# Optimization experiments

Hardware: AMD Instinct MI355X
Metric: run time of the kernel (lower is better)

Reference implementation:

```python
import jax, jax.numpy as jnp
import numpy as np

H, KV, HD = 16, 8, 128           # heads, kv heads, head_dim
THETA, EPS = 1.0e6, 1e-6         # rope theta, rmsnorm eps
QMAX = 127.0                     # symmetric int8


def qdq(x):
    """Symmetric int8 fake quant-dequant along last dim (per-token / per-out-channel)."""
    s = jnp.maximum(jnp.max(jnp.abs(x), axis=-1, keepdims=True) / QMAX, 1e-8)
    q = jnp.clip(jnp.round(x / s), -QMAX, QMAX) * s
    return x + jax.lax.stop_gradient(q - x)  # STE


def rms_norm(x, w):
    v = jnp.mean(jnp.square(x.astype(jnp.float32)), axis=-1, keepdims=True)
    return (x.astype(jnp.float32) * jax.lax.rsqrt(v + EPS)).astype(x.dtype) * w


def rotate_half(x):
    x1, x2 = jnp.split(x, 2, axis=-1)
    return jnp.concatenate([-x2, x1], axis=-1)


def setup_inputs() -> dict:
    key = jax.random.key(0)
    ks = jax.random.split(key, 6)
    B, S, D = 1, 2048, 2048
    return {
        "hidden_states": jax.random.normal(ks[0], (B, S, D), jnp.float32),
        "Wq": jax.random.normal(ks[1], (H * HD, D), jnp.float32) * 0.02,
        "Wk": jax.random.normal(ks[2], (KV * HD, D), jnp.float32) * 0.02,
        "Wv": jax.random.normal(ks[3], (KV * HD, D), jnp.float32) * 0.02,
        "Wo": jax.random.normal(ks[4], (D, H * HD), jnp.float32) * 0.02,
        "q_norm_w": jnp.ones((HD,), jnp.float32),
        "k_norm_w": jnp.ones((HD,), jnp.float32),
        "position_ids": jnp.arange(S, dtype=jnp.int32)[None, :],
    }


def reference(hidden_states, Wq, Wk, Wv, Wo, q_norm_w, k_norm_w, position_ids):
    B, S, D = hidden_states.shape
    xq = qdq(hidden_states)                                  # per-token act quant (shared input)
    q = (xq @ qdq(Wq).T).reshape(B, S, H, HD).transpose(0, 2, 1, 3)   # [B,H,S,hd]
    k = (xq @ qdq(Wk).T).reshape(B, S, KV, HD).transpose(0, 2, 1, 3)  # [B,KV,S,hd]
    v = (xq @ qdq(Wv).T).reshape(B, S, KV, HD).transpose(0, 2, 1, 3)

    q = rms_norm(q, q_norm_w)
    k = rms_norm(k, k_norm_w)

    # rotary embeddings
    inv = 1.0 / (THETA ** (jnp.arange(0, HD, 2, dtype=jnp.float32) / HD))
    freqs = position_ids.astype(jnp.float32)[..., None] * inv          # [B,S,hd/2]
    emb = jnp.concatenate([freqs, freqs], axis=-1)                     # [B,S,hd]
    cos = jnp.cos(emb)[:, None].astype(q.dtype)                        # [B,1,S,hd]
    sin = jnp.sin(emb)[:, None].astype(q.dtype)
    q = q * cos + rotate_half(q) * sin
    k = k * cos + rotate_half(k) * sin

    # qkt_matmul.quant_x1 / quant_x2
    q = qdq(q)
    k = qdq(k)

    # GQA repeat
    g = H // KV
    k = jnp.repeat(k, g, axis=1)
    v = jnp.repeat(v, g, axis=1)

    scores = jnp.einsum("bhqd,bhkd->bhqk", q, k) * (HD ** -0.5)       # [B,H,S,S]
    causal = jnp.tril(jnp.ones((S, S), bool))
    scores = jnp.where(causal[None, None], scores, jnp.float32(-1e9))
    p = jax.nn.softmax(scores.astype(jnp.float32), axis=-1).astype(q.dtype)

    # pv_matmul.quant_x1 / quant_x2
    p = qdq(p)
    v = qdq(v)
    attn = jnp.einsum("bhqk,bhkd->bhqd", p, v)                        # [B,H,S,hd]
    attn = attn.transpose(0, 2, 1, 3).reshape(B, S, H * HD)
    return qdq(attn) @ qdq(Wo).T
```

## Files before the change

kernel.cpp:

```cpp
#include <hip/hip_runtime.h>
#include <math.h>

#define NH 16
#define NKV 8
#define HDIM 128
#define SEQ 2048
#define DMODEL 2048

typedef int   v4i __attribute__((ext_vector_type(4)));
typedef float v4f __attribute__((ext_vector_type(4)));
typedef _Float16 v8h __attribute__((ext_vector_type(8)));

static constexpr float SM_SCALE = 0.08838834764831843f;

#define GLOBP(p) (__attribute__((address_space(1))) void*)(p)
#define LDSP(p)  (__attribute__((address_space(3))) void*)(p)
#define ASYNC16(g, l) __builtin_amdgcn_global_load_lds(GLOBP(g), LDSP(l), 16, 0, 0)


__device__ __forceinline__ unsigned short f2h_bits(float x) {
    _Float16 h = (_Float16)x;
    return __builtin_bit_cast(unsigned short, h);
}

__global__ __launch_bounds__(256) void quant_rope_k(const float* __restrict__ hidden,
        const float* __restrict__ Wq, const float* __restrict__ Wk,
        const float* __restrict__ Wv, const float* __restrict__ Wo,
        const int* __restrict__ pos_ids,
        signed char* __restrict__ out, float* __restrict__ scale,
        float* __restrict__ ct, float* __restrict__ st) {
    int p = blockIdx.x;
    if (p >= 512) {
        int t = (p - 512) * 4 + (threadIdx.x >> 6);
        int fi = threadIdx.x & 63;
        float inv = 1.0f / (float)pow(1.0e6, (double)fi / 64.0);
        float fr = (float)pos_ids[t] * inv;
        float sn, c;
        sincosf(fr, &sn, &c);
        ct[t * 64 + fi] = c;
        st[t * 64 + fi] = sn;
        return;
    }
    int row0g = p * 16;
    const float* in; int lr0;
    if (row0g < 2048)      { in = hidden; lr0 = row0g; }
    else if (row0g < 4096) { in = Wq; lr0 = row0g - 2048; }
    else if (row0g < 5120) { in = Wk; lr0 = row0g - 4096; }
    else if (row0g < 6144) { in = Wv; lr0 = row0g - 5120; }
    else                   { in = Wo; lr0 = row0g - 6144; }
    const int cols = 2048;
    int tid = threadIdx.x;
    __shared__ float srow[16];
    int r = tid >> 4, l16 = tid & 15;
    const float4* x4 = (const float4*)(in + (size_t)(lr0 + r) * cols);
    float amax = 0.f;
    for (int c4 = l16; c4 < (cols >> 2); c4 += 16) {
        float4 v = x4[c4];
        amax = fmaxf(amax, fmaxf(fmaxf(fabsf(v.x), fabsf(v.y)),
                                 fmaxf(fabsf(v.z), fabsf(v.w))));
    }
#pragma unroll
    for (int m = 1; m <= 8; m <<= 1) amax = fmaxf(amax, __shfl_xor(amax, m));
    if (l16 == 0) {
        float s = fmaxf(amax / 127.0f, 1e-8f);
        srow[r] = s;
        scale[row0g + r] = s;
    }
    __syncthreads();
    int total = (cols >> 4) * 16;
    size_t obase = (size_t)p * 32768;
    for (int idx = tid; idx < total; idx += 256) {
        int f = idx >> 6, q = (idx >> 4) & 3, rr = idx & 15;
        const float* src = in + (size_t)(lr0 + rr) * cols + f * 64 + q * 16;
        float s = srow[rr];
        unsigned int wds[4];
#pragma unroll
        for (int g = 0; g < 4; ++g) {
            float4 v = *(const float4*)(src + g * 4);
            int b0 = (int)fminf(fmaxf(rintf(v.x / s), -127.f), 127.f);
            int b1 = (int)fminf(fmaxf(rintf(v.y / s), -127.f), 127.f);
            int b2 = (int)fminf(fmaxf(rintf(v.z / s), -127.f), 127.f);
            int b3 = (int)fminf(fmaxf(rintf(v.w / s), -127.f), 127.f);
            wds[g] = (b0 & 255) | ((b1 & 255) << 8) | ((b2 & 255) << 16) | ((b3 & 255) << 24);
        }
        *(uint4*)(out + obase + (size_t)idx * 16) =
            make_uint4(wds[0], wds[1], wds[2], wds[3]);
    }
}

__global__ __launch_bounds__(256) void row_quant_red_k(const float* __restrict__ attn2,
        const float* __restrict__ pp, const float* __restrict__ zb,
        signed char* __restrict__ out, float* __restrict__ scale) {
    int row0 = blockIdx.x * 16;
    int tid = threadIdx.x;
    __shared__ float srow[16];
    __shared__ float4 spvt[16][17];
    {
        int r = tid >> 4, h = tid & 15;
        int row = row0 + r;
        int t32 = row >> 6, rr = row & 63;
        const float2* zb2 = (const float2*)zb;
        float2 a0 = zb2[(((size_t)h * 32 + t32) * 2 + 0) * 64 + rr];
        float2 a1 = zb2[(((size_t)h * 32 + t32) * 2 + 1) * 64 + rr];
        float M = fmaxf(a0.x, a1.x);
        float w0 = __expf(a0.x - M), w1 = __expf(a1.x - M);
        float Zt = a0.y * w0 + a1.y * w1;
        float spv = fmaxf((1.0f / Zt) / 127.0f, 1e-8f);
        spvt[r][h] = make_float4(w0, w1, spv, 0.f);
    }
    __syncthreads();
    int r = tid >> 4, l16 = tid & 15;
    int row = row0 + r;
    const float4* x4 = (const float4*)(attn2 + (size_t)row * 2048);
    size_t ppr = ((size_t)(row >> 6) * 64 + (row & 63)) * 128;
    float amax = 0.f;
    for (int c4 = l16; c4 < 512; c4 += 16) {
        float4 v = x4[c4];
        int h = c4 >> 5;
        int j = (c4 & 31) * 4;
        float4 pv = *(const float4*)&pp[(size_t)h * 32 * 64 * 128 + ppr + j];
        float4 wz = spvt[r][h];
        v.x = (v.x * wz.x + pv.x * wz.y) * wz.z;
        v.y = (v.y * wz.x + pv.y * wz.y) * wz.z;
        v.z = (v.z * wz.x + pv.z * wz.y) * wz.z;
        v.w = (v.w * wz.x + pv.w * wz.y) * wz.z;
        amax = fmaxf(amax, fmaxf(fmaxf(fabsf(v.x), fabsf(v.y)),
                                 fmaxf(fabsf(v.z), fabsf(v.w))));
    }
#pragma unroll
    for (int m = 1; m <= 8; m <<= 1) amax = fmaxf(amax, __shfl_xor(amax, m));
    if (l16 == 0) {
        float s = fmaxf(amax / 127.0f, 1e-8f);
        srow[r] = s;
        scale[row0 + r] = s;
    }
    __syncthreads();
    size_t obase = ((size_t)(row0 >> 4) * 32) << 10;
    for (int idx = tid; idx < 2048; idx += 256) {
        int f = idx >> 6, q = (idx >> 4) & 3, rr16 = idx & 15;
        int rowb = row0 + rr16;
        int colb = f * 64 + q * 16;
        const float* src = attn2 + (size_t)rowb * 2048 + colb;
        float s = srow[rr16];
        int h = f >> 1;
        float4 wz = spvt[rr16][h];
        size_t ppb = (size_t)h * 32 * 64 * 128
                   + ((size_t)(rowb >> 6) * 64 + (rowb & 63)) * 128 + (colb & 127);
        unsigned int wds[4];
#pragma unroll
        for (int g = 0; g < 4; ++g) {
            float4 v = *(const float4*)(src + g * 4);
            float4 pv = *(const float4*)&pp[ppb + g * 4];
            v.x = (v.x * wz.x + pv.x * wz.y) * wz.z;
            v.y = (v.y * wz.x + pv.y * wz.y) * wz.z;
            v.z = (v.z * wz.x + pv.z * wz.y) * wz.z;
            v.w = (v.w * wz.x + pv.w * wz.y) * wz.z;
            int b0 = (int)fminf(fmaxf(rintf(v.x / s), -127.f), 127.f);
            int b1 = (int)fminf(fmaxf(rintf(v.y / s), -127.f), 127.f);
            int b2 = (int)fminf(fmaxf(rintf(v.z / s), -127.f), 127.f);
            int b3 = (int)fminf(fmaxf(rintf(v.w / s), -127.f), 127.f);
            wds[g] = (b0 & 255) | ((b1 & 255) << 8) | ((b2 & 255) << 16) | ((b3 & 255) << 24);
        }
        *(uint4*)(out + obase + (size_t)idx * 16) =
            make_uint4(wds[0], wds[1], wds[2], wds[3]);
    }
}

__global__ __launch_bounds__(256, 3) void gemm_o_k(const signed char* __restrict__ A,
        const float* __restrict__ sa, const signed char* __restrict__ B,
        const float* __restrict__ sb, float* __restrict__ C, int M, int N, int K) {
    __shared__ __align__(16) signed char lsA[3][8192];
    __shared__ __align__(16) signed char lsB[3][4096];
    int tid = threadIdx.x;
    int w = tid >> 6, l = tid & 63;
    int wr = w >> 1, wc = w & 1;
    int lrow = l & 15;
    int m0 = blockIdx.y * 128, n0 = blockIdx.x * 64;
    int kb6 = K >> 6;
    v4i acc[4][2];
#pragma unroll
    for (int i = 0; i < 4; ++i)
#pragma unroll
        for (int j = 0; j < 2; ++j) acc[i][j] = (v4i){0, 0, 0, 0};

    auto stage = [&](int buf, int k6) {
#pragma unroll
        for (int a = 0; a < 2; ++a) {
            int f = a * 4 + w;
            ASYNC16(A + (((size_t)(((m0 >> 4) + f) * kb6 + k6)) << 10) + l * 16,
                    lsA[buf] + f * 1024);
        }
        ASYNC16(B + (((size_t)(((n0 >> 4) + w) * kb6 + k6)) << 10) + l * 16,
                lsB[buf] + w * 1024);
    };

    stage(0, 0);
    if (kb6 > 1) {
        stage(1, 1);
        asm volatile("s_waitcnt vmcnt(3)" ::: "memory");
    } else {
        asm volatile("s_waitcnt vmcnt(0)" ::: "memory");
    }
    __builtin_amdgcn_s_barrier();
    for (int t = 0; t < kb6; ++t) {
        if (t + 2 < kb6) stage((t + 2) % 3, t + 2);
        int cur = t % 3;
        v4i af[4], bf[2];
#pragma unroll
        for (int i = 0; i < 4; ++i) af[i] = *(const v4i*)(lsA[cur] + (wr * 4 + i) * 1024 + l * 16);
#pragma unroll
        for (int j = 0; j < 2; ++j) bf[j] = *(const v4i*)(lsB[cur] + (wc * 2 + j) * 1024 + l * 16);
#pragma unroll
        for (int i = 0; i < 4; ++i)
#pragma unroll
            for (int j = 0; j < 2; ++j)
                acc[i][j] = __builtin_amdgcn_mfma_i32_16x16x64_i8(af[i], bf[j], acc[i][j], 0, 0, 0);
        if (t + 2 < kb6) asm volatile("s_waitcnt vmcnt(3)" ::: "memory");
        else             asm volatile("s_waitcnt vmcnt(0)" ::: "memory");
        __builtin_amdgcn_s_barrier();
    }
    int r0 = m0 + wr * 64, c0 = n0 + wc * 32;
    int lg = l >> 4;
    float sbv[2];
#pragma unroll
    for (int j = 0; j < 2; ++j) sbv[j] = sb[c0 + j * 16 + lrow];
#pragma unroll
    for (int i = 0; i < 4; ++i) {
        float4 s4 = *(const float4*)(sa + r0 + i * 16 + lg * 4);
        float sav[4] = {s4.x, s4.y, s4.z, s4.w};
#pragma unroll
        for (int j = 0; j < 2; ++j) {
#pragma unroll
            for (int reg = 0; reg < 4; ++reg) {
                int rr = r0 + i * 16 + lg * 4 + reg;
                C[(size_t)rr * N + c0 + j * 16 + lrow] = (float)acc[i][j][reg] * (sav[reg] * sbv[j]);
            }
        }
    }
}

__global__ __launch_bounds__(256, 2) void gemm_qkv_k(const signed char* __restrict__ A,
        const float* __restrict__ sa, const signed char* __restrict__ B,
        const float* __restrict__ sb,
        const float* __restrict__ qw, const float* __restrict__ kw,
        const float* __restrict__ ct, const float* __restrict__ st,
        signed char* __restrict__ q_i8, float* __restrict__ sq,
        signed char* __restrict__ k_i8, float* __restrict__ sk,
        unsigned short* __restrict__ vtT) {
    __shared__ __align__(16) char smem[68608];
    signed char (*lsA)[8192] = (signed char(*)[8192])smem;
    signed char (*lsB)[8192] = (signed char(*)[8192])(smem + 24576);
    float (*tile)[132] = (float(*)[132])smem;
    float* srow = (float*)(smem + 67584);
    int tid = threadIdx.x;
    int w = tid >> 6, l = tid & 63;
    int wr = w >> 1, wc = w & 1;
    int lrow = l & 15, lg = l >> 4;
    int m0 = blockIdx.y * 128, n0 = blockIdx.x * 128;
    const int kb6 = 32;
    v4i acc[4][4];
#pragma unroll
    for (int i = 0; i < 4; ++i)
#pragma unroll
        for (int j = 0; j < 4; ++j) acc[i][j] = (v4i){0, 0, 0, 0};

    auto stage = [&](int buf, int k6) {
#pragma unroll
        for (int a = 0; a < 2; ++a) {
            int f = a * 4 + w;
            ASYNC16(A + (((size_t)(((m0 >> 4) + f) * kb6 + k6)) << 10) + l * 16,
                    lsA[buf] + f * 1024);
            ASYNC16(B + (((size_t)(((n0 >> 4) + f) * kb6 + k6)) << 10) + l * 16,
                    lsB[buf] + f * 1024);
        }
    };

    stage(0, 0);
    stage(1, 1);
    asm volatile("s_waitcnt vmcnt(4)" ::: "memory");
    __builtin_amdgcn_s_barrier();
    for (int t = 0; t < kb6; ++t) {
        if (t + 2 < kb6) stage((t + 2) % 3, t + 2);
        int cur = t % 3;
        v4i af[4], bf[4];
#pragma unroll
        for (int i = 0; i < 4; ++i) af[i] = *(const v4i*)(lsA[cur] + (wr * 4 + i) * 1024 + l * 16);
#pragma unroll
        for (int j = 0; j < 4; ++j) bf[j] = *(const v4i*)(lsB[cur] + (wc * 4 + j) * 1024 + l * 16);
#pragma unroll
        for (int i = 0; i < 4; ++i)
#pragma unroll
            for (int j = 0; j < 4; ++j)
                acc[i][j] = __builtin_amdgcn_mfma_i32_16x16x64_i8(af[i], bf[j], acc[i][j], 0, 0, 0);
        if (t + 2 < kb6) asm volatile("s_waitcnt vmcnt(4)" ::: "memory");
        else             asm volatile("s_waitcnt vmcnt(0)" ::: "memory");
        __builtin_amdgcn_s_barrier();
    }
    {
        int c0 = n0 + wc * 64;
        float sbv[4];
#pragma unroll
        for (int j = 0; j < 4; ++j) sbv[j] = sb[c0 + j * 16 + lrow];
#pragma unroll
        for (int i = 0; i < 4; ++i) {
            float4 s4 = *(const float4*)(sa + m0 + wr * 64 + i * 16 + lg * 4);
            float sav[4] = {s4.x, s4.y, s4.z, s4.w};
#pragma unroll
            for (int j = 0; j < 4; ++j)
#pragma unroll
                for (int reg = 0; reg < 4; ++reg)
                    tile[wr * 64 + i * 16 + lg * 4 + reg][wc * 64 + j * 16 + lrow] =
                        (float)acc[i][j][reg] * (sav[reg] * sbv[j]);
        }
    }
    __syncthreads();
    int slot = n0 >> 7;
    if (slot < 24) {
        const float* wn = (slot < 16) ? qw : kw;
        signed char* dst8 = (slot < 16) ? q_i8 + (size_t)slot * (SEQ * 128)
                                        : k_i8 + (size_t)(slot - 16) * (SEQ * 128);
        float* sdst = (slot < 16) ? sq + (size_t)slot * SEQ : sk + (size_t)(slot - 16) * SEQ;
        float wn0 = wn[l], wn1 = wn[l + 64];
        for (int it = 0; it < 32; ++it) {
            int tl = it * 4 + w;
            int t = m0 + tl;
            float x0 = tile[tl][l];
            float x1 = tile[tl][l + 64];
            float ss = x0 * x0 + x1 * x1;
#pragma unroll
            for (int m = 1; m <= 32; m <<= 1) ss += __shfl_xor(ss, m);
            float rs = 1.0f / sqrtf(ss / 128.0f + 1e-6f);
            x0 = (x0 * rs) * wn0;
            x1 = (x1 * rs) * wn1;
            float cth = ct[t * 64 + l];
            float sth = st[t * 64 + l];
            float nx0 = x0 * cth - x1 * sth;
            float nx1 = x1 * cth + x0 * sth;
            float amax = fmaxf(fabsf(nx0), fabsf(nx1));
#pragma unroll
            for (int m = 1; m <= 32; m <<= 1) amax = fmaxf(amax, __shfl_xor(amax, m));
            float s = fmaxf(amax / 127.0f, 1e-8f);
            float q0 = fminf(fmaxf(rintf(nx0 / s), -127.f), 127.f);
            float q1 = fminf(fmaxf(rintf(nx1 / s), -127.f), 127.f);
            size_t ta0 = (size_t)(((t >> 4) * 2) << 10)
                       + (size_t)((((l >> 4) & 3) << 8) + ((t & 15) << 4) + (l & 15));
            dst8[ta0] = (signed char)(int)q0;
            dst8[ta0 + 1024] = (signed char)(int)q1;
            if (l == 0) sdst[t] = s;
        }
    } else {
        int kv = slot - 24;
        for (int it = 0; it < 32; ++it) {
            int tl = it * 4 + w;
            float x0 = tile[tl][l];
            float x1 = tile[tl][l + 64];
            float amax = fmaxf(fabsf(x0), fabsf(x1));
#pragma unroll
            for (int m = 1; m <= 32; m <<= 1) amax = fmaxf(amax, __shfl_xor(amax, m));
            if (l == 0) srow[tl] = fmaxf(amax / 127.0f, 1e-8f);
        }
        __syncthreads();
        int d = tid >> 1, th = (tid & 1) * 32;
        size_t base = (size_t)kv * (SEQ * 128);
#pragma unroll
        for (int kbl = 0; kbl < 2; ++kbl) {
            int kb = (m0 >> 6) + kbl;
#pragma unroll
            for (int j = 0; j < 32; j += 2) {
                int t64 = th + j;
                int tg = kbl * 64 + t64;
                float s0 = srow[tg], s1 = srow[tg + 1];
                float a = fminf(fmaxf(rintf(tile[tg][d] / s0), -127.f), 127.f) * s0;
                float b = fminf(fmaxf(rintf(tile[tg + 1][d] / s1), -127.f), 127.f) * s1;
                unsigned int ua = f2h_bits(a), ub = f2h_bits(b);
                int off = kb * 8192 + ((d >> 4) * 2 + ((t64 >> 5) & 1)) * 512
                        + (((d & 15) + (((t64 >> 3) & 3) << 4)) << 3) + (t64 & 7);
                *(unsigned int*)(vtT + base + off) = ua | (ub << 16);
            }
        }
    }
}

__global__ __launch_bounds__(256, 2) void attn_k(const signed char* __restrict__ q_i8,
        const float* __restrict__ sq, const signed char* __restrict__ k_i8,
        const float* __restrict__ sk, const unsigned short* __restrict__ vtT,
        float* __restrict__ attn2, float* __restrict__ pp, float* __restrict__ zb) {
    __shared__ __align__(16) unsigned short vlds[2][8192];
    __shared__ __align__(16) signed char klds[8192];
    __shared__ __align__(16) unsigned short plds[4096];
    int bx = blockIdx.x, hp = blockIdx.y;
    int qb = 31 - (bx >> 1), c = bx & 1;
    int q0 = qb * 64;
    int hsp = (qb + 2) >> 1;
    int kb0 = c ? hsp : 0;
    int kb1 = c ? (qb + 1) : hsp;
    int tid = threadIdx.x, w = tid >> 6, l = tid & 63;
    int lrow = l & 15, lg = l >> 4;
    int h0 = hp * 2, h1 = h0 + 1;

    if (kb0 >= kb1) {
        if (lrow == 0) {
            float2* zb2 = (float2*)zb;
            size_t zA = (((size_t)h0 * 32 + qb) * 2 + c) * 64;
            size_t zB = (((size_t)h1 * 32 + qb) * 2 + c) * 64;
#pragma unroll
            for (int reg = 0; reg < 4; ++reg) {
                zb2[zA + w * 16 + lg * 4 + reg] = make_float2(-1e30f, 0.f);
                zb2[zB + w * 16 + lg * 4 + reg] = make_float2(-1e30f, 0.f);
            }
        }
        return;
    }

    const signed char* qtA = q_i8 + (size_t)h0 * (SEQ * 128)
                           + ((size_t)((((q0 >> 4) + w) * 2)) << 10) + l * 16;
    const signed char* qtB = qtA + (size_t)(SEQ * 128);
    v4i qfA0 = *(const v4i*)(qtA), qfA1 = *(const v4i*)(qtA + 1024);
    v4i qfB0 = *(const v4i*)(qtB), qfB1 = *(const v4i*)(qtB + 1024);
    float4 sA = *(const float4*)(sq + (size_t)h0 * SEQ + q0 + w * 16 + lg * 4);
    float4 sB = *(const float4*)(sq + (size_t)h1 * SEQ + q0 + w * 16 + lg * 4);
    float sqrA[4] = {sA.x, sA.y, sA.z, sA.w};
    float sqrB[4] = {sB.x, sB.y, sB.z, sB.w};

    const signed char* kbase = k_i8 + (size_t)hp * (SEQ * 128);
    const float* skb = sk + (size_t)hp * SEQ;
    const unsigned short* vt = vtT + (size_t)hp * (SEQ * 128);

    auto issueV = [&](int kb) {
        unsigned short* vb = &vlds[kb & 1][0];
#pragma unroll
        for (int a = 0; a < 4; ++a) {
            int fv = a * 4 + w;
            ASYNC16(vt + (size_t)kb * 8192 + fv * 512 + l * 8, vb + fv * 512);
        }
    };
    auto issueK = [&](int kb) {
#pragma unroll
        for (int a = 0; a < 2; ++a) {
            int f = a * 4 + w;
            ASYNC16(kbase + ((size_t)(kb * 8 + f) << 10) + l * 16, klds + f * 1024);
        }
    };

    v4f accA[8], accB[8];
#pragma unroll
    for (int jd = 0; jd < 8; ++jd) {
        accA[jd] = (v4f){0.f, 0.f, 0.f, 0.f};
        accB[jd] = (v4f){0.f, 0.f, 0.f, 0.f};
    }
    float ztA[4] = {0.f, 0.f, 0.f, 0.f};
    float ztB[4] = {0.f, 0.f, 0.f, 0.f};
    float mA[4], mB[4];
#pragma unroll
    for (int r = 0; r < 4; ++r) { mA[r] = -1e30f; mB[r] = -1e30f; }

    issueK(kb0);
    issueV(kb0);
    asm volatile("s_waitcnt vmcnt(0)" ::: "memory");
    __builtin_amdgcn_s_barrier();

    for (int kb = kb0; kb < kb1; ++kb) {
        int k0 = kb * 64;
        if (kb + 1 < kb1) issueV(kb + 1);
        v4i ka[8];
#pragma unroll
        for (int f = 0; f < 8; ++f)
            ka[f] = *(const v4i*)(klds + f * 1024 + l * 16);
        float skc[4];
#pragma unroll
        for (int j = 0; j < 4; ++j) skc[j] = skb[k0 + j * 16 + lrow];
        v4i sciA[4], sciB[4];
#pragma unroll
        for (int j = 0; j < 4; ++j) {
            v4i z = {0, 0, 0, 0};
            v4i tA = __builtin_amdgcn_mfma_i32_16x16x64_i8(qfA0, ka[j * 2], z, 0, 0, 0);
            sciA[j] = __builtin_amdgcn_mfma_i32_16x16x64_i8(qfA1, ka[j * 2 + 1], tA, 0, 0, 0);
            v4i tB = __builtin_amdgcn_mfma_i32_16x16x64_i8(qfB0, ka[j * 2], z, 0, 0, 0);
            sciB[j] = __builtin_amdgcn_mfma_i32_16x16x64_i8(qfB1, ka[j * 2 + 1], tB, 0, 0, 0);
        }
        __builtin_amdgcn_s_barrier();
        if (kb + 1 < kb1) issueK(kb + 1);
        float svA[4][4], svB[4][4];
        float tmA[4], tmB[4];
#pragma unroll
        for (int reg = 0; reg < 4; ++reg) { tmA[reg] = -1e30f; tmB[reg] = -1e30f; }
#pragma unroll
        for (int reg = 0; reg < 4; ++reg) {
            int r = q0 + w * 16 + lg * 4 + reg;
#pragma unroll
            for (int j = 0; j < 4; ++j) {
                int cc = j * 16 + lrow;
                bool ok = (k0 + cc <= r);
                float ss = skc[j] * SM_SCALE;
                svA[reg][j] = ok ? ((float)sciA[j][reg] * sqrA[reg]) * ss : -1e30f;
                svB[reg][j] = ok ? ((float)sciB[j][reg] * sqrB[reg]) * ss : -1e30f;
                tmA[reg] = fmaxf(tmA[reg], svA[reg][j]);
                tmB[reg] = fmaxf(tmB[reg], svB[reg][j]);
            }
        }
#pragma unroll
        for (int reg = 0; reg < 4; ++reg) {
#pragma unroll
            for (int mask = 1; mask <= 8; mask <<= 1) {
                tmA[reg] = fmaxf(tmA[reg], __shfl_xor(tmA[reg], mask));
                tmB[reg] = fmaxf(tmB[reg], __shfl_xor(tmB[reg], mask));
            }
        }
        float efA[4], efB[4];
#pragma unroll
        for (int reg = 0; reg < 4; ++reg) {
            float mnA = fmaxf(mA[reg], tmA[reg]);
            efA[reg] = __expf(mA[reg] - mnA);
            mA[reg] = mnA;
            ztA[reg] *= efA[reg];
            float mnB = fmaxf(mB[reg], tmB[reg]);
            efB[reg] = __expf(mB[reg] - mnB);
            mB[reg] = mnB;
            ztB[reg] *= efB[reg];
        }
        v4f efvA = {efA[0], efA[1], efA[2], efA[3]};
        v4f efvB = {efB[0], efB[1], efB[2], efB[3]};
#pragma unroll
        for (int jd = 0; jd < 8; ++jd) {
            accA[jd] *= efvA;
            accB[jd] *= efvB;
        }
#pragma unroll
        for (int reg = 0; reg < 4; ++reg) {
            int rq = lg * 4 + reg;
#pragma unroll
            for (int j = 0; j < 4; ++j) {
                int cc = j * 16 + lrow;
                float pd = 0.f;
                float sv = svA[reg][j];
                if (sv > -5e29f) {
                    float e = __expf(sv - mA[reg]);
                    ztA[reg] += e;
                    pd = fminf(rintf(127.0f * e), 127.f);
                }
                plds[(w * 2 + (cc >> 5)) * 512 + (rq + 16 * ((cc >> 3) & 3)) * 8 + (cc & 7)] =
                    f2h_bits(pd);
            }
        }
        v8h pfA0 = *(const v8h*)(plds + (w * 2 + 0) * 512 + l * 8);
        v8h pfA1 = *(const v8h*)(plds + (w * 2 + 1) * 512 + l * 8);
#pragma unroll
        for (int reg = 0; reg < 4; ++reg) {
            int rq = lg * 4 + reg;
#pragma unroll
            for (int j = 0; j < 4; ++j) {
                int cc = j * 16 + lrow;
                float pd = 0.f;
                float sv = svB[reg][j];
                if (sv > -5e29f) {
                    float e = __expf(sv - mB[reg]);
                    ztB[reg] += e;
                    pd = fminf(rintf(127.0f * e), 127.f);
                }
                plds[(w * 2 + (cc >> 5)) * 512 + (rq + 16 * ((cc >> 3) & 3)) * 8 + (cc & 7)] =
                    f2h_bits(pd);
            }
        }
        v8h pfB0 = *(const v8h*)(plds + (w * 2 + 0) * 512 + l * 8);
        v8h pfB1 = *(const v8h*)(plds + (w * 2 + 1) * 512 + l * 8);
        const unsigned short* vb = &vlds[kb & 1][0];
#pragma unroll
        for (int jd = 0; jd < 8; ++jd) {
            v8h vh0 = *(const v8h*)(vb + (jd * 2 + 0) * 512 + l * 8);
            v8h vh1 = *(const v8h*)(vb + (jd * 2 + 1) * 512 + l * 8);
            v4f tA = accA[jd];
            tA = __builtin_amdgcn_mfma_f32_16x16x32_f16(pfA0, vh0, tA, 0, 0, 0);
            tA = __builtin_amdgcn_mfma_f32_16x16x32_f16(pfA1, vh1, tA, 0, 0, 0);
            accA[jd] = tA;
            v4f tB = accB[jd];
            tB = __builtin_amdgcn_mfma_f32_16x16x32_f16(pfB0, vh0, tB, 0, 0, 0);
            tB = __builtin_amdgcn_mfma_f32_16x16x32_f16(pfB1, vh1, tB, 0, 0, 0);
            accB[jd] = tB;
        }
        asm volatile("s_waitcnt vmcnt(0)" ::: "memory");
        __builtin_amdgcn_s_barrier();
    }
#pragma unroll
    for (int reg = 0; reg < 4; ++reg) {
#pragma unroll
        for (int mask = 1; mask <= 8; mask <<= 1) {
            ztA[reg] += __shfl_xor(ztA[reg], mask);
            ztB[reg] += __shfl_xor(ztB[reg], mask);
        }
    }
    if (c == 0) {
#pragma unroll
        for (int jd = 0; jd < 8; ++jd)
#pragma unroll
            for (int reg = 0; reg < 4; ++reg) {
                int r = q0 + w * 16 + lg * 4 + reg;
                attn2[(size_t)r * DMODEL + h0 * HDIM + jd * 16 + lrow] = accA[jd][reg];
                attn2[(size_t)r * DMODEL + h1 * HDIM + jd * 16 + lrow] = accB[jd][reg];
            }
    } else {
#pragma unroll
        for (int jd = 0; jd < 8; ++jd)
#pragma unroll
            for (int reg = 0; reg < 4; ++reg) {
                int rr = w * 16 + lg * 4 + reg;
                pp[(((size_t)h0 * 32 + qb) * 64 + rr) * 128 + jd * 16 + lrow] = accA[jd][reg];
                pp[(((size_t)h1 * 32 + qb) * 64 + rr) * 128 + jd * 16 + lrow] = accB[jd][reg];
            }
    }
    if (lrow == 0) {
        float2* zb2 = (float2*)zb;
        size_t zA = (((size_t)h0 * 32 + qb) * 2 + c) * 64;
        size_t zB = (((size_t)h1 * 32 + qb) * 2 + c) * 64;
#pragma unroll
        for (int reg = 0; reg < 4; ++reg) {
            zb2[zA + w * 16 + lg * 4 + reg] = make_float2(mA[reg], ztA[reg]);
            zb2[zB + w * 16 + lg * 4 + reg] = make_float2(mB[reg], ztB[reg]);
        }
    }
}

extern "C" void kernel_launch(void* const* d_in, const int* in_sizes, int n_in,
                              void* d_out, int out_size, void* d_ws, size_t ws_size,
                              hipStream_t stream) {
    (void)in_sizes; (void)n_in; (void)out_size; (void)ws_size;
    const float* hidden = (const float*)d_in[0];
    const float* Wq = (const float*)d_in[1];
    const float* Wk = (const float*)d_in[2];
    const float* Wv = (const float*)d_in[3];
    const float* Wo = (const float*)d_in[4];
    const float* qw = (const float*)d_in[5];
    const float* kw = (const float*)d_in[6];
    const int* pos = (const int*)d_in[7];
    float* out = (float*)d_out;
    char* ws = (char*)d_ws;

    const size_t MB = 1024 * 1024;
    signed char* x_i8  = (signed char*)(ws);
    signed char* wq_i8 = (signed char*)(ws + 4 * MB);
    signed char* wo_i8 = (signed char*)(ws + 12 * MB);
    signed char* q_i8  = (signed char*)(ws + 16 * MB);
    signed char* k_i8  = (signed char*)(ws + 20 * MB);
    float* sx  = (float*)(ws + 22 * MB);
    float* swq = sx + 2048;
    float* swo = sx + 6144;
    float* sq  = sx + 8192;
    float* sk  = sq + NH * SEQ;
    float* sa  = sk + NKV * SEQ;
    float* ct  = (float*)(ws + 22 * MB + 512 * 1024);
    float* st  = (float*)(ws + 22 * MB + 1024 * 1024);
    unsigned short* vtT = (unsigned short*)(ws + 24 * MB);
    float* zb    = (float*)(ws + 28 * MB);
    float* attn2 = (float*)(ws + 30 * MB);
    float* pp    = (float*)(ws + 46 * MB);
    signed char* a_i8 = x_i8;

    quant_rope_k<<<1024, 256, 0, stream>>>(hidden, Wq, Wk, Wv, Wo, pos, x_i8, sx, ct, st);

    gemm_qkv_k<<<dim3(32, 16), 256, 0, stream>>>(x_i8, sx, wq_i8, swq, qw, kw, ct, st,
                                                 q_i8, sq, k_i8, sk, vtT);

    attn_k<<<dim3(64, 8), 256, 0, stream>>>(q_i8, sq, k_i8, sk, vtT, attn2, pp, zb);

    row_quant_red_k<<<128, 256, 0, stream>>>(attn2, pp, zb, a_i8, sa);
    gemm_o_k<<<dim3(32, 16), 256, 0, stream>>>(a_i8, sa, wo_i8, swo, out, 2048, 2048, 2048);
}
```

Before: 179.2 us.

## Split attention work so each wave handles one head and half the query rows

Each attention block now covers 32 query rows instead of 64, with waves 0-1 handling the first head of the KV pair and waves 2-3 the second. Previously each wave computed both heads over 16 rows. The grid doubles to 128x8 blocks and per-wave register use roughly halves (one accumulator set, one P tile). This targets occupancy, register pressure and load balance, but the same K/V tile is now loaded into LDS by twice as many blocks, doubling K/V traffic per query.

Result: faster. 171.1 us (median of 2 runs) (-4.5%).

```diff
diff --git a/kernel.cpp b/kernel.cpp
--- a/kernel.cpp
+++ b/kernel.cpp
@@ -389,38 +389,34 @@
     __shared__ __align__(16) signed char klds[8192];
     __shared__ __align__(16) unsigned short plds[4096];
     int bx = blockIdx.x, hp = blockIdx.y;
-    int qb = 31 - (bx >> 1), c = bx & 1;
-    int q0 = qb * 64;
+    int qs = 63 - (bx >> 1), c = bx & 1;
+    int qb = qs >> 1;
+    int q0s = qs * 32;
     int hsp = (qb + 2) >> 1;
     int kb0 = c ? hsp : 0;
     int kb1 = c ? (qb + 1) : hsp;
     int tid = threadIdx.x, w = tid >> 6, l = tid & 63;
     int lrow = l & 15, lg = l >> 4;
-    int h0 = hp * 2, h1 = h0 + 1;
+    int hh = hp * 2 + (w >> 1);
+    int wrow = (w & 1) * 16;
+    int rrb = (qs & 1) * 32 + wrow;
 
     if (kb0 >= kb1) {
         if (lrow == 0) {
             float2* zb2 = (float2*)zb;
-            size_t zA = (((size_t)h0 * 32 + qb) * 2 + c) * 64;
-            size_t zB = (((size_t)h1 * 32 + qb) * 2 + c) * 64;
-#pragma unroll
-            for (int reg = 0; reg < 4; ++reg) {
-                zb2[zA + w * 16 + lg * 4 + reg] = make_float2(-1e30f, 0.f);
-                zb2[zB + w * 16 + lg * 4 + reg] = make_float2(-1e30f, 0.f);
-            }
+            size_t z = (((size_t)hh * 32 + qb) * 2 + c) * 64;
+#pragma unroll
+            for (int reg = 0; reg < 4; ++reg)
+                zb2[z + rrb + lg * 4 + reg] = make_float2(-1e30f, 0.f);
         }
         return;
     }
 
-    const signed char* qtA = q_i8 + (size_t)h0 * (SEQ * 128)
-                           + ((size_t)((((q0 >> 4) + w) * 2)) << 10) + l * 16;
-    const signed char* qtB = qtA + (size_t)(SEQ * 128);
-    v4i qfA0 = *(const v4i*)(qtA), qfA1 = *(const v4i*)(qtA + 1024);
-    v4i qfB0 = *(const v4i*)(qtB), qfB1 = *(const v4i*)(qtB + 1024);
-    float4 sA = *(const float4*)(sq + (size_t)h0 * SEQ + q0 + w * 16 + lg * 4);
-    float4 sB = *(const float4*)(sq + (size_t)h1 * SEQ + q0 + w * 16 + lg * 4);
-    float sqrA[4] = {sA.x, sA.y, sA.z, sA.w};
-    float sqrB[4] = {sB.x, sB.y, sB.z, sB.w};
+    const signed char* qt = q_i8 + (size_t)hh * (SEQ * 128)
+                          + ((size_t)((qs * 2 + (w & 1)) * 2) << 10) + l * 16;
+    v4i qf0 = *(const v4i*)(qt), qf1 = *(const v4i*)(qt + 1024);
+    float4 s4 = *(const float4*)(sq + (size_t)hh * SEQ + q0s + wrow + lg * 4);
+    float sqr[4] = {s4.x, s4.y, s4.z, s4.w};
 
     const signed char* kbase = k_i8 + (size_t)hp * (SEQ * 128);
     const float* skb = sk + (size_t)hp * SEQ;
@@ -442,17 +438,13 @@
         }
     };
 
-    v4f accA[8], accB[8];
-#pragma unroll
-    for (int jd = 0; jd < 8; ++jd) {
-        accA[jd] = (v4f){0.f, 0.f, 0.f, 0.f};
-        accB[jd] = (v4f){0.f, 0.f, 0.f, 0.f};
-    }
-    float ztA[4] = {0.f, 0.f, 0.f, 0.f};
-    float ztB[4] = {0.f, 0.f, 0.f, 0.f};
-    float mA[4], mB[4];
-#pragma unroll
-    for (int r = 0; r < 4; ++r) { mA[r] = -1e30f; mB[r] = -1e30f; }
+    v4f acc[8];
+#pragma unroll
+    for (int jd = 0; jd < 8; ++jd) acc[jd] = (v4f){0.f, 0.f, 0.f, 0.f};
+    float zt[4] = {0.f, 0.f, 0.f, 0.f};
+    float mr[4];
+#pragma unroll
+    for (int r = 0; r < 4; ++r) mr[r] = -1e30f;
 
     issueK(kb0);
     issueV(kb0);
@@ -469,62 +461,48 @@
         float skc[4];
 #pragma unroll
         for (int j = 0; j < 4; ++j) skc[j] = skb[k0 + j * 16 + lrow];
-        v4i sciA[4], sciB[4];
+        v4i sci[4];
 #pragma unroll
         for (int j = 0; j < 4; ++j) {
             v4i z = {0, 0, 0, 0};
-            v4i tA = __builtin_amdgcn_mfma_i32_16x16x64_i8(qfA0, ka[j * 2], z, 0, 0, 0);
-            sciA[j] = __builtin_amdgcn_mfma_i32_16x16x64_i8(qfA1, ka[j * 2 + 1], tA, 0, 0, 0);
-            v4i tB = __builtin_amdgcn_mfma_i32_16x16x64_i8(qfB0, ka[j * 2], z, 0, 0, 0);
-            sciB[j] = __builtin_amdgcn_mfma_i32_16x16x64_i8(qfB1, ka[j * 2 + 1], tB, 0, 0, 0);
+            v4i t0 = __builtin_amdgcn_mfma_i32_16x16x64_i8(qf0, ka[j * 2], z, 0, 0, 0);
+            sci[j] = __builtin_amdgcn_mfma_i32_16x16x64_i8(qf1, ka[j * 2 + 1], t0, 0, 0, 0);
         }
         __builtin_amdgcn_s_barrier();
         if (kb + 1 < kb1) issueK(kb + 1);
-        float svA[4][4], svB[4][4];
-        float tmA[4], tmB[4];
-#pragma unroll
-        for (int reg = 0; reg < 4; ++reg) { tmA[reg] = -1e30f; tmB[reg] = -1e30f; }
+        float sv[4][4];
+        float tm[4];
+#pragma unroll
+        for (int reg = 0; reg < 4; ++reg) tm[reg] = -1e30f;
 #pragma unroll
         for (int reg = 0; reg < 4; ++reg) {
-            int r = q0 + w * 16 + lg * 4 + reg;
+            int r = q0s + wrow + lg * 4 + reg;
 #pragma unroll
             for (int j = 0; j < 4; ++j) {
                 int cc = j * 16 + lrow;
                 bool ok = (k0 + cc <= r);
                 float ss = skc[j] * SM_SCALE;
-                svA[reg][j] = ok ? ((float)sciA[j][reg] * sqrA[reg]) * ss : -1e30f;
-                svB[reg][j] = ok ? ((float)sciB[j][reg] * sqrB[reg]) * ss : -1e30f;
-                tmA[reg] = fmaxf(tmA[reg], svA[reg][j]);
-                tmB[reg] = fmaxf(tmB[reg], svB[reg][j]);
+                sv[reg][j] = ok ? ((float)sci[j][reg] * sqr[reg]) * ss : -1e30f;
+                tm[reg] = fmaxf(tm[reg], sv[reg][j]);
             }
         }
 #pragma unroll
         for (int reg = 0; reg < 4; ++reg) {
 #pragma unroll
-            for (int mask = 1; mask <= 8; mask <<= 1) {
-                tmA[reg] = fmaxf(tmA[reg], __shfl_xor(tmA[reg], mask));
-                tmB[reg] = fmaxf(tmB[reg], __shfl_xor(tmB[reg], mask));
-            }
-        }
-        float efA[4], efB[4];
+            for (int mask = 1; mask <= 8; mask <<= 1)
+                tm[reg] = fmaxf(tm[reg], __shfl_xor(tm[reg], mask));
+        }
+        float ef[4];
 #pragma unroll
         for (int reg = 0; reg < 4; ++reg) {
-            float mnA = fmaxf(mA[reg], tmA[reg]);
-            efA[reg] = __expf(mA[reg] - mnA);
-            mA[reg] = mnA;
-            ztA[reg] *= efA[reg];
-            float mnB = fmaxf(mB[reg], tmB[reg]);
-            efB[reg] = __expf(mB[reg] - mnB);
-            mB[reg] = mnB;
-            ztB[reg] *= efB[reg];
-        }
-        v4f efvA = {efA[0], efA[1], efA[2], efA[3]};
-        v4f efvB = {efB[0], efB[1], efB[2], efB[3]};
-#pragma unroll
-        for (int jd = 0; jd < 8; ++jd) {
-            accA[jd] *= efvA;
-            accB[jd] *= efvB;
-        }
+            float mn = fmaxf(mr[reg], tm[reg]);
+            ef[reg] = __expf(mr[reg] - mn);
+            mr[reg] = mn;
+            zt[reg] *= ef[reg];
+        }
+        v4f efv = {ef[0], ef[1], ef[2], ef[3]};
+#pragma unroll
+        for (int jd = 0; jd < 8; ++jd) acc[jd] *= efv;
 #pragma unroll
         for (int reg = 0; reg < 4; ++reg) {
             int rq = lg * 4 + reg;
@@ -532,50 +510,27 @@
             for (int j = 0; j < 4; ++j) {
                 int cc = j * 16 + lrow;
                 float pd = 0.f;
-                float sv = svA[reg][j];
-                if (sv > -5e29f) {
-                    float e = __expf(sv - mA[reg]);
-                    ztA[reg] += e;
+                float s = sv[reg][j];
+                if (s > -5e29f) {
+                    float e = __expf(s - mr[reg]);
+                    zt[reg] += e;
                     pd = fminf(rintf(127.0f * e), 127.f);
                 }
                 plds[(w * 2 + (cc >> 5)) * 512 + (rq + 16 * ((cc >> 3) & 3)) * 8 + (cc & 7)] =
                     f2h_bits(pd);
             }
         }
-        v8h pfA0 = *(const v8h*)(plds + (w * 2 + 0) * 512 + l * 8);
-        v8h pfA1 = *(const v8h*)(plds + (w * 2 + 1) * 512 + l * 8);
-#pragma unroll
-        for (int reg = 0; reg < 4; ++reg) {
-            int rq = lg * 4 + reg;
-#pragma unroll
-            for (int j = 0; j < 4; ++j) {
-                int cc = j * 16 + lrow;
-                float pd = 0.f;
-                float sv = svB[reg][j];
-                if (sv > -5e29f) {
-                    float e = __expf(sv - mB[reg]);
-                    ztB[reg] += e;
-                    pd = fminf(rintf(127.0f * e), 127.f);
-                }
-                plds[(w * 2 + (cc >> 5)) * 512 + (rq + 16 * ((cc >> 3) & 3)) * 8 + (cc & 7)] =
-                    f2h_bits(pd);
-            }
-        }
-        v8h pfB0 = *(const v8h*)(plds + (w * 2 + 0) * 512 + l * 8);
-        v8h pfB1 = *(const v8h*)(plds + (w * 2 + 1) * 512 + l * 8);
+        v8h pf0 = *(const v8h*)(plds + (w * 2 + 0) * 512 + l * 8);
+        v8h pf1 = *(const v8h*)(plds + (w * 2 + 1) * 512 + l * 8);
         const unsigned short* vb = &vlds[kb & 1][0];
 #pragma unroll
         for (int jd = 0; jd < 8; ++jd) {
             v8h vh0 = *(const v8h*)(vb + (jd * 2 + 0) * 512 + l * 8);
             v8h vh1 = *(const v8h*)(vb + (jd * 2 + 1) * 512 + l * 8);
-            v4f tA = accA[jd];
-            tA = __builtin_amdgcn_mfma_f32_16x16x32_f16(pfA0, vh0, tA, 0, 0, 0);
-            tA = __builtin_amdgcn_mfma_f32_16x16x32_f16(pfA1, vh1, tA, 0, 0, 0);
-            accA[jd] = tA;
-            v4f tB = accB[jd];
-            tB = __builtin_amdgcn_mfma_f32_16x16x32_f16(pfB0, vh0, tB, 0, 0, 0);
-            tB = __builtin_amdgcn_mfma_f32_16x16x32_f16(pfB1, vh1, tB, 0, 0, 0);
-            accB[jd] = tB;
+            v4f t = acc[jd];
+            t = __builtin_amdgcn_mfma_f32_16x16x32_f16(pf0, vh0, t, 0, 0, 0);
+            t = __builtin_amdgcn_mfma_f32_16x16x32_f16(pf1, vh1, t, 0, 0, 0);
+            acc[jd] = t;
         }
         asm volatile("s_waitcnt vmcnt(0)" ::: "memory");
         __builtin_amdgcn_s_barrier();
@@ -583,39 +538,32 @@
 #pragma unroll
     for (int reg = 0; reg < 4; ++reg) {
 #pragma unroll
-        for (int mask = 1; mask <= 8; mask <<= 1) {
-            ztA[reg] += __shfl_xor(ztA[reg], mask);
-            ztB[reg] += __shfl_xor(ztB[reg], mask);
-        }
+        for (int mask = 1; mask <= 8; mask <<= 1)
+            zt[reg] += __shfl_xor(zt[reg], mask);
     }
     if (c == 0) {
 #pragma unroll
         for (int jd = 0; jd < 8; ++jd)
 #pragma unroll
             for (int reg = 0; reg < 4; ++reg) {
-                int r = q0 + w * 16 + lg * 4 + reg;
-                attn2[(size_t)r * DMODEL + h0 * HDIM + jd * 16 + lrow] = accA[jd][reg];
-                attn2[(size_t)r * DMODEL + h1 * HDIM + jd * 16 + lrow] = accB[jd][reg];
+                int r = q0s + wrow + lg * 4 + reg;
+                attn2[(size_t)r * DMODEL + hh * HDIM + jd * 16 + lrow] = acc[jd][reg];
             }
     } else {
 #pragma unroll
         for (int jd = 0; jd < 8; ++jd)
 #pragma unroll
             for (int reg = 0; reg < 4; ++reg) {
-                int rr = w * 16 + lg * 4 + reg;
-                pp[(((size_t)h0 * 32 + qb) * 64 + rr) * 128 + jd * 16 + lrow] = accA[jd][reg];
-                pp[(((size_t)h1 * 32 + qb) * 64 + rr) * 128 + jd * 16 + lrow] = accB[jd][reg];
+                int rr = rrb + lg * 4 + reg;
+                pp[(((size_t)hh * 32 + qb) * 64 + rr) * 128 + jd * 16 + lrow] = acc[jd][reg];
             }
     }
     if (lrow == 0) {
         float2* zb2 = (float2*)zb;
-        size_t zA = (((size_t)h0 * 32 + qb) * 2 + c) * 64;
-        size_t zB = (((size_t)h1 * 32 + qb) * 2 + c) * 64;
-#pragma unroll
-        for (int reg = 0; reg < 4; ++reg) {
-            zb2[zA + w * 16 + lg * 4 + reg] = make_float2(mA[reg], ztA[reg]);
-            zb2[zB + w * 16 + lg * 4 + reg] = make_float2(mB[reg], ztB[reg]);
-        }
+        size_t z = (((size_t)hh * 32 + qb) * 2 + c) * 64;
+#pragma unroll
+        for (int reg = 0; reg < 4; ++reg)
+            zb2[z + rrb + lg * 4 + reg] = make_float2(mr[reg], zt[reg]);
     }
 }
 
@@ -659,7 +607,7 @@
     gemm_qkv_k<<<dim3(32, 16), 256, 0, stream>>>(x_i8, sx, wq_i8, swq, qw, kw, ct, st,
                                                  q_i8, sq, k_i8, sk, vtT);
 
-    attn_k<<<dim3(64, 8), 256, 0, stream>>>(q_i8, sq, k_i8, sk, vtT, attn2, pp, zb);
+    attn_k<<<dim3(128, 8), 256, 0, stream>>>(q_i8, sq, k_i8, sk, vtT, attn2, pp, zb);
 
     row_quant_red_k<<<128, 256, 0, stream>>>(attn2, pp, zb, a_i8, sa);
     gemm_o_k<<<dim3(32, 16), 256, 0, stream>>>(a_i8, sa, wo_i8, swo, out, 2048, 2048, 2048);
```
